# Optimization experiments

Hardware: AMD Instinct MI355X
Metric: run time of the kernel (lower is better)

The kernel has to match this reference:

```python
import jax, jax.numpy as jnp
import numpy as np

K_DEFAULT = 1000.0  # torch.eye(3).fill_(1000.) fills ALL 9 entries, not just the diagonal
THRESH = 3.0
PENALTY = 10000.0


def setup_inputs() -> dict:
    key = jax.random.key(0)
    k1, k2, k3, k4, k5 = jax.random.split(key, 5)
    N, H, D, C = 2048, 128, 7, 64
    return {
        "start_state": jax.random.normal(k1, (1, D), dtype=jnp.float32),
        "state_batch": jax.random.normal(k2, (N, H, D), dtype=jnp.float32),
        "normals": jax.random.normal(k3, (C, 3), dtype=jnp.float32),
        "jac": jax.random.normal(k4, (C, 3, D), dtype=jnp.float32),
        "forces": jax.random.uniform(k5, (C,), dtype=jnp.float32),
    }


def reference(start_state, state_batch, normals, jac, forces):
    # k_c: torch.eye(3).fill_(1000.) => every entry 1000
    k_c = jnp.full((3, 3), K_DEFAULT, dtype=state_batch.dtype)
    # relative joint state: [N, H, 7]
    sb = state_batch[:, :, :7] - start_state[:, :7]
    # out[c, k] = normals[c, :] @ k_c @ jac[c, :, :]  -> [C, 7]
    out = jnp.einsum('ci,ij,cjk->ck', normals, k_c, jac)
    # deltas[n, h, c] = out[c, :] . sb[n, h, :]  (replaces the double Python loop)
    deltas = jnp.einsum('ck,nhk->nhc', out, sb)
    # fi[n, h] = sum_c (forces[c] + deltas[n, h, c])
    fi = jnp.sum(forces[None, None, :] + deltas, axis=2)
    cost = jnp.where(fi > THRESH, jnp.asarray(PENALTY, fi.dtype), jnp.zeros((), fi.dtype))
    return cost
```

## Files before the change

kernel.cpp:

```cpp
#include <hip/hip_runtime.h>


#define FTC_D 7

__global__ __launch_bounds__(64) void ftc_setup_kernel(
    const float* __restrict__ start_state,
    const float* __restrict__ normals,
    const float* __restrict__ jac,
    const float* __restrict__ forces,
    double* __restrict__ wb)
{
    const int c = threadIdx.x;
    double sn = (double)normals[c * 3 + 0]
              + (double)normals[c * 3 + 1]
              + (double)normals[c * 3 + 2];
    double vals[8];
    #pragma unroll
    for (int k = 0; k < FTC_D; ++k) {
        double tk = (double)jac[c * 21 + 0 * 7 + k]
                  + (double)jac[c * 21 + 1 * 7 + k]
                  + (double)jac[c * 21 + 2 * 7 + k];
        vals[k] = 1000.0 * sn * tk;
    }
    vals[7] = (double)forces[c];

    #pragma unroll
    for (int off = 32; off > 0; off >>= 1) {
        #pragma unroll
        for (int k = 0; k < 8; ++k)
            vals[k] += __shfl_xor(vals[k], off, 64);
    }

    if (c == 0) {
        double b = vals[7];
        #pragma unroll
        for (int k = 0; k < FTC_D; ++k) b -= vals[k] * (double)start_state[k];
        #pragma unroll
        for (int k = 0; k < FTC_D; ++k) wb[k] = vals[k];
        wb[7] = b;
    }
}

__global__ __launch_bounds__(256) void ftc_main_kernel(
    const float* __restrict__ state_batch,
    const double* __restrict__ wb,
    float* __restrict__ out,
    int nquad)
{
    double w0 = wb[0], w1 = wb[1], w2 = wb[2], w3 = wb[3];
    double w4 = wb[4], w5 = wb[5], w6 = wb[6];
    double bias = wb[7];

    int t = blockIdx.x * 256 + threadIdx.x;
    if (t < nquad) {
        const float4* p = (const float4*)(state_batch + (size_t)t * 28);
        float v[28];
        float4* vv = (float4*)v;
        #pragma unroll
        for (int j = 0; j < 7; ++j) vv[j] = p[j];

        float4 o;
        float* ov = &o.x;
        #pragma unroll
        for (int r = 0; r < 4; ++r) {
            const float* s = v + r * 7;
            double fi = bias;
            fi = fma((double)s[0], w0, fi);
            fi = fma((double)s[1], w1, fi);
            fi = fma((double)s[2], w2, fi);
            fi = fma((double)s[3], w3, fi);
            fi = fma((double)s[4], w4, fi);
            fi = fma((double)s[5], w5, fi);
            fi = fma((double)s[6], w6, fi);
            ov[r] = (fi > 3.0) ? 10000.0f : 0.0f;
        }
        ((float4*)out)[t] = o;
    }
}

extern "C" void kernel_launch(void* const* d_in, const int* in_sizes, int n_in,
                              void* d_out, int out_size, void* d_ws, size_t ws_size,
                              hipStream_t stream) {
    const float* start_state = (const float*)d_in[0];
    const float* state_batch = (const float*)d_in[1];
    const float* normals     = (const float*)d_in[2];
    const float* jac         = (const float*)d_in[3];
    const float* forces      = (const float*)d_in[4];
    float* out = (float*)d_out;
    double* wb = (double*)d_ws;

    int ntot  = in_sizes[1] / FTC_D;
    int nquad = ntot / 4;
    int grid  = (nquad + 255) / 256;

    ftc_setup_kernel<<<1, 64, 0, stream>>>(start_state, normals, jac, forces, wb);
    ftc_main_kernel<<<grid, 256, 0, stream>>>(state_batch, wb, out, nquad);
}
```

Measured before the change: 67.73 us.

## Fuse weight setup into main kernel, recomputing reduction per wavefront

Merges the single-block setup kernel into the main streaming kernel. Each 64-lane wavefront now recomputes the contact-weight reduction from the small normals/jac/forces inputs with shuffles, while its state_batch loads are already issued. This removes one kernel launch, the serial dependency between the two kernels, and the workspace round trip. In exchange every wavefront does redundant double-precision shuffle reductions and holds more live registers.

```diff
diff --git a/kernel.cpp b/kernel.cpp
--- a/kernel.cpp
+++ b/kernel.cpp
@@ -3,14 +3,26 @@
 
 #define FTC_D 7
 
-__global__ __launch_bounds__(64) void ftc_setup_kernel(
+__global__ __launch_bounds__(256) void ftc_fused_kernel(
     const float* __restrict__ start_state,
+    const float* __restrict__ state_batch,
     const float* __restrict__ normals,
     const float* __restrict__ jac,
     const float* __restrict__ forces,
-    double* __restrict__ wb)
+    float* __restrict__ out,
+    int nquad)
 {
-    const int c = threadIdx.x;
+    const int t = blockIdx.x * 256 + threadIdx.x;
+
+    float v[28];
+    if (t < nquad) {
+        const float4* p = (const float4*)(state_batch + (size_t)t * 28);
+        float4* vv = (float4*)v;
+        #pragma unroll
+        for (int j = 0; j < 7; ++j) vv[j] = p[j];
+    }
+
+    const int c = threadIdx.x & 63;
     double sn = (double)normals[c * 3 + 0]
               + (double)normals[c * 3 + 1]
               + (double)normals[c * 3 + 2];
@@ -31,47 +43,20 @@
             vals[k] += __shfl_xor(vals[k], off, 64);
     }
 
-    if (c == 0) {
-        double b = vals[7];
-        #pragma unroll
-        for (int k = 0; k < FTC_D; ++k) b -= vals[k] * (double)start_state[k];
-        #pragma unroll
-        for (int k = 0; k < FTC_D; ++k) wb[k] = vals[k];
-        wb[7] = b;
-    }
-}
+    double bias = vals[7];
+    #pragma unroll
+    for (int k = 0; k < FTC_D; ++k) bias -= vals[k] * (double)start_state[k];
 
-__global__ __launch_bounds__(256) void ftc_main_kernel(
-    const float* __restrict__ state_batch,
-    const double* __restrict__ wb,
-    float* __restrict__ out,
-    int nquad)
-{
-    double w0 = wb[0], w1 = wb[1], w2 = wb[2], w3 = wb[3];
-    double w4 = wb[4], w5 = wb[5], w6 = wb[6];
-    double bias = wb[7];
-
-    int t = blockIdx.x * 256 + threadIdx.x;
     if (t < nquad) {
-        const float4* p = (const float4*)(state_batch + (size_t)t * 28);
-        float v[28];
-        float4* vv = (float4*)v;
-        #pragma unroll
-        for (int j = 0; j < 7; ++j) vv[j] = p[j];
-
         float4 o;
         float* ov = &o.x;
         #pragma unroll
         for (int r = 0; r < 4; ++r) {
             const float* s = v + r * 7;
             double fi = bias;
-            fi = fma((double)s[0], w0, fi);
-            fi = fma((double)s[1], w1, fi);
-            fi = fma((double)s[2], w2, fi);
-            fi = fma((double)s[3], w3, fi);
-            fi = fma((double)s[4], w4, fi);
-            fi = fma((double)s[5], w5, fi);
-            fi = fma((double)s[6], w6, fi);
+            #pragma unroll
+            for (int k = 0; k < FTC_D; ++k)
+                fi = fma((double)s[k], vals[k], fi);
             ov[r] = (fi > 3.0) ? 10000.0f : 0.0f;
         }
         ((float4*)out)[t] = o;
@@ -87,12 +72,11 @@
     const float* jac         = (const float*)d_in[3];
     const float* forces      = (const float*)d_in[4];
     float* out = (float*)d_out;
-    double* wb = (double*)d_ws;
 
     int ntot  = in_sizes[1] / FTC_D;
     int nquad = ntot / 4;
     int grid  = (nquad + 255) / 256;
 
-    ftc_setup_kernel<<<1, 64, 0, stream>>>(start_state, normals, jac, forces, wb);
-    ftc_main_kernel<<<grid, 256, 0, stream>>>(state_batch, wb, out, nquad);
+    ftc_fused_kernel<<<grid, 256, 0, stream>>>(
+        start_state, state_batch, normals, jac, forces, out, nquad);
 }
```

Result: no change. 68.26 us (+0.8%).
